# Kernel tuning notes

Measured on AMD Instinct MI355X. Metric: run time of the kernel, lower is better.

The kernel has to match this reference:

```python
import jax, jax.numpy as jnp
import numpy as np

K = 1023   # kernel_size == embedding_dim
H = 16     # out_channels (filters per sample)
E = 256    # num_embeddings
T = 8      # num_tokens
CC = 0.25  # commitment cost
EPS = np.float32(np.finfo(np.float32).eps)
DN = ('NCH', 'OIH', 'NCH')


def setup_inputs() -> dict:
    key = jax.random.key(0)
    ks = jax.random.split(key, 10)
    B, C, L = 8, 1, 8184
    D_ff = 2 * E
    X = jax.random.normal(ks[0], (B, C, L), jnp.float32)
    embedding = jax.random.uniform(ks[1], (E, K), jnp.float32, -1.0 / E, 1.0 / E)
    ffn_w1 = jax.random.normal(ks[2], (E, D_ff), jnp.float32) * 0.02
    ffn_b1 = jnp.zeros((D_ff,), jnp.float32)
    ffn_w2 = jax.random.normal(ks[3], (D_ff, E), jnp.float32) * 0.02
    ffn_b2 = jnp.zeros((E,), jnp.float32)
    ln_g = jnp.ones((E,), jnp.float32)
    ln_b = jnp.zeros((E,), jnp.float32)
    cls_w = jax.random.normal(ks[4], (E, 10), jnp.float32) * 0.02
    cls_b = jnp.zeros((10,), jnp.float32)
    return dict(X=X, embedding=embedding, ffn_w1=ffn_w1, ffn_b1=ffn_b1,
                ffn_w2=ffn_w2, ffn_b2=ffn_b2, ln_g=ln_g, ln_b=ln_b,
                cls_w=cls_w, cls_b=cls_b)


def _autocov(f):
    # f: [..., K]. FFT-based autocovariance of hann-windowed, max-normalized frame.
    n = f.shape[-1]
    fmax = jnp.max(jnp.abs(f), axis=-1, keepdims=True)
    fmax = jnp.where(fmax == 0, EPS, fmax)
    win = 0.5 * (1.0 - jnp.cos(2.0 * jnp.pi * jnp.arange(n, dtype=jnp.float32) / n))
    xw = f * win / fmax
    spec = jnp.abs(jnp.fft.rfft(xw, n=n) ** 2)   # |rfft(x)^2| == |rfft(x)|^2
    return jnp.fft.ifftshift(jnp.fft.irfft(spec, n=n), axes=-1)


def reference(X, embedding, ffn_w1, ffn_b1, ffn_w2, ffn_b2, ln_g, ln_b, cls_w, cls_b):
    B, C, L = X.shape
    # ---- encoder: extract frames at fixed linspace positions, autocovariance ----
    Lp = ((L + K - 1) // K) * K          # PadForConv(zero) length (no-op here)
    end = Lp - K - 1 - K
    positions = jnp.linspace(0.0, float(end), H).astype(jnp.int32)
    idx = positions[:, None] + jnp.arange(K)          # (H, K)
    frames = X[:, :, idx]                             # (B, C, H, K) gather
    Z = _autocov(jnp.transpose(frames, (0, 2, 1, 3)))  # (B, H, C, K)
    # ---- VQ: pairwise distances + argmin + codebook lookup ----
    flat = Z.reshape(-1, K)                           # (B*H*C, K)
    d = (jnp.sum(flat ** 2, axis=1, keepdims=True)
         + jnp.sum(embedding ** 2, axis=1)
         - 2.0 * flat @ embedding.T)                  # (B*H*C, E)
    codes = jnp.argmin(d, axis=1)
    enc = jax.nn.one_hot(codes, E, dtype=flat.dtype)
    quant = (enc @ embedding).reshape(Z.shape)
    sg = jax.lax.stop_gradient
    e_loss = jnp.mean((sg(quant) - Z) ** 2)
    q_loss = jnp.mean((quant - sg(Z)) ** 2)
    vq_loss = q_loss + CC * e_loss
    quant_st = Z + sg(quant - Z)                      # straight-through
    avg = jnp.mean(enc, axis=0)
    perplexity = jnp.exp(-jnp.sum(avg * jnp.log(avg + EPS)))
    # ---- decoder: every sample's filter bank convolved with the whole batch ----
    fmerged = quant_st.reshape(B * H, C, K)           # merge per-sample banks
    out = jax.lax.conv_general_dilated(X, fmerged, (1,), 'SAME',
                                       dimension_numbers=DN)  # (B, B*H, L)
    out = out.reshape(B, B, H, L)                     # (batch b, filter-sample i, k, L)
    sq = (out - X[:, None, :, :]) ** 2                # C==1 broadcast
    # sum_i mean_k mse_{b,l} == mean over (b,k,l) then sum over i
    recon_loss = jnp.sum(jnp.mean(sq, axis=(0, 2, 3)))
    # ---- project: conv with codebook as filters ----
    pfilt = jnp.broadcast_to(embedding[:, None, :], (E, C, K))
    proj = jax.lax.conv_general_dilated(X, pfilt, (1,), 'VALID',
                                        dimension_numbers=DN)  # (B, E, Lo)
    Lo = proj.shape[-1]
    pad = ((Lo + T - 1) // T) * T - Lo                # PadForConv(mean)
    m = jnp.mean(proj, axis=-1, keepdims=True)
    proj = jnp.concatenate([proj, jnp.broadcast_to(m, (B, E, pad))], axis=-1)
    # ---- classify ----
    x = proj.reshape(B, E, T, -1).transpose(0, 2, 3, 1)  # (B, T, t, E)
    x = jnp.max(x, axis=2)                               # (B, T, E)
    mu = jnp.mean(x, axis=-1, keepdims=True)
    var = jnp.var(x, axis=-1, keepdims=True)
    xn = (x - mu) / jnp.sqrt(var + 1e-5) * ln_g + ln_b
    hdd = jax.nn.relu(xn @ ffn_w1 + ffn_b1) @ ffn_w2 + ffn_b2
    feat = jnp.mean(hdd, axis=1)                         # (B, E)
    logits = feat @ cls_w + cls_b
    return (logits, vq_loss, recon_loss, perplexity)
```

## Files before the change

kernel.cpp:

```cpp
#include <hip/hip_runtime.h>

#define KK 1023
#define LL 8184
#define LO 7162
#define XPS 10240
#define EPSF 1.1920928955078125e-07f
#define NEG_INF (-3.4028234663852886e+38f)

typedef short bf16x8 __attribute__((ext_vector_type(8)));
typedef float f32x4 __attribute__((ext_vector_type(4)));

__device__ __constant__ int c_pos[16] = {0,409,818,1227,1636,2045,2454,2863,
                                         3273,3682,4091,4500,4909,5318,5727,6137};

__device__ __forceinline__ unsigned short f2bf(float f) {
    unsigned u = __float_as_uint(f);
    unsigned r = (u + 0x7FFFu + ((u >> 16) & 1u)) >> 16;
    return (unsigned short)r;
}
__device__ __forceinline__ int fenc(float f) {
    int u = __float_as_int(f);
    return u >= 0 ? u : (~u) ^ 0x80000000;
}
__device__ __forceinline__ float fdec(int k) {
    int u = k >= 0 ? k : ~(k ^ 0x80000000);
    return __int_as_float(u);
}
__device__ __forceinline__ void gl2lds16(const void* g, void* l) {
    __builtin_amdgcn_global_load_lds(
        (const __attribute__((address_space(1))) void*)g,
        (__attribute__((address_space(3))) void*)l, 16, 0, 0);
}

__global__ __launch_bounds__(256) void k_pa(const float* __restrict__ X,
                                            const float* __restrict__ emb,
                                            unsigned short* __restrict__ Xpad,
                                            unsigned short* __restrict__ Xodd,
                                            unsigned short* __restrict__ Ebf,
                                            float* __restrict__ Etf,
                                            float* __restrict__ enorm,
                                            int* __restrict__ hist,
                                            int* __restrict__ cmax,
                                            float* __restrict__ Z) {
    __shared__ __align__(16) float xw[2048];
    __shared__ float red[256];
    const int q = blockIdx.x;
    const int tid = threadIdx.x;
    if (q < 256) {
        const int fi = q >> 1, half = q & 1;
        const int b = fi >> 4, h = fi & 15;
        const float* xp = X + b * LL + c_pos[h];
        float lmax = 0.f;
        for (int j = tid; j < KK; j += 256) {
            float v = xp[j];
            xw[j] = v;
            lmax = fmaxf(lmax, fabsf(v));
        }
        red[tid] = lmax;
        __syncthreads();
        for (int off = 128; off; off >>= 1) {
            if (tid < off) red[tid] = fmaxf(red[tid], red[tid + off]);
            __syncthreads();
        }
        float fmx = red[0];
        if (fmx == 0.f) fmx = EPSF;
        __syncthreads();
        for (int j = tid; j < KK; j += 256) {
            float v = xw[j];
            float win = 0.5f * (1.0f - cosf(6.28318530717958647692f * (float)j / 1023.0f));
            float w = v * win / fmx;
            xw[j] = w;
            xw[j + KK] = w;
        }
        __syncthreads();

        if (tid < 128) {
            const int m = half * 512 + 4 * tid;
            const int mh = m >> 1;
            const int mq4 = mh >> 1;
            const float2* X2 = (const float2*)xw;
            const float4* X4 = (const float4*)xw;
            float a0 = 0.f, a1 = 0.f, a2 = 0.f, a3 = 0.f;
            float2 W0 = X2[mh], W1 = X2[mh + 1], W2 = X2[mh + 2], W3 = X2[mh + 3];
            for (int jh = 0; jh < 510; jh += 2) {
                float4 nw = X4[mq4 + (jh >> 1) + 2];
                float4 xj = X4[jh >> 1];
                a0 = fmaf(xj.x, W0.x, a0);
                a0 = fmaf(xj.y, W0.y, a0);
                a0 = fmaf(xj.z, W1.x, a0);
                a0 = fmaf(xj.w, W1.y, a0);
                a1 = fmaf(xj.x, W0.y, a1);
                a1 = fmaf(xj.y, W1.x, a1);
                a1 = fmaf(xj.z, W1.y, a1);
                a1 = fmaf(xj.w, W2.x, a1);
                a2 = fmaf(xj.x, W1.x, a2);
                a2 = fmaf(xj.y, W1.y, a2);
                a2 = fmaf(xj.z, W2.x, a2);
                a2 = fmaf(xj.w, W2.y, a2);
                a3 = fmaf(xj.x, W1.y, a3);
                a3 = fmaf(xj.y, W2.x, a3);
                a3 = fmaf(xj.z, W2.y, a3);
                a3 = fmaf(xj.w, W3.x, a3);
                W0 = W2; W1 = W3;
                W2 = make_float2(nw.x, nw.y);
                W3 = make_float2(nw.z, nw.w);
            }
            {
                float2 xj = X2[510];
                a0 = fmaf(xj.x, W0.x, a0);
                a0 = fmaf(xj.y, W0.y, a0);
                a1 = fmaf(xj.x, W0.y, a1);
                a1 = fmaf(xj.y, W1.x, a1);
                a2 = fmaf(xj.x, W1.x, a2);
                a2 = fmaf(xj.y, W1.y, a2);
                a3 = fmaf(xj.x, W1.y, a3);
                a3 = fmaf(xj.y, W2.x, a3);
            }
            float xt = xw[1022];
            a0 = fmaf(xt, W1.x, a0);
            a1 = fmaf(xt, W1.y, a1);
            a2 = fmaf(xt, W2.x, a2);
            a3 = fmaf(xt, W2.y, a3);

            float* zrow = Z + fi * KK;
            float av[4] = {a0, a1, a2, a3};
#pragma unroll
            for (int qq = 0; qq < 4; ++qq) {
                int mmq = m + qq;
                if (mmq < KK) {
                    int i0 = mmq + 512; if (i0 >= KK) i0 -= KK;
                    zrow[i0] = av[qq];
                }
            }
        }
    } else if (q < 288) {
        const int qq = q - 256;
        const int b = qq >> 2, seg = qq & 3;
        for (int i = seg * 2560 + tid; i < (seg + 1) * 2560; i += 256) {
            unsigned short v = 0, vo = 0;
            if (i >= 512 && i < 512 + LL) v = f2bf(X[b * LL + (i - 512)]);
            const int i1 = i + 1;
            if (i1 >= 512 && i1 < 512 + LL) vo = f2bf(X[b * LL + (i1 - 512)]);
            Xpad[b * XPS + i] = v;
            Xodd[b * XPS + i] = vo;
        }
    } else if (q < 544) {
        const int e = q - 288;
        const float* er = emb + e * KK;
        float nrm = 0.f;
        for (int k = tid; k < 1024; k += 256) {
            float v = (k < KK) ? er[k] : 0.f;
            Ebf[e * 1024 + k] = (k < KK) ? f2bf(v) : (unsigned short)0;
            Etf[(k >> 2) * 1024 + e * 4 + (k & 3)] = v;
            nrm = fmaf(v, v, nrm);
        }
        red[tid] = nrm;
        __syncthreads();
        for (int off = 128; off; off >>= 1) {
            if (tid < off) red[tid] += red[tid + off];
            __syncthreads();
        }
        if (tid == 0) enorm[e] = red[0];
    } else {
        const int i = (q - 544) * 256 + tid;
        cmax[i] = INT_MIN;
        if (q == 544) hist[tid] = 0;
    }
}

__global__ __launch_bounds__(256, 4) void kA(const float* __restrict__ Z,
                                             const float4* __restrict__ Et4,
                                             const float* __restrict__ enorm,
                                             const float* __restrict__ emb,
                                             int* __restrict__ codes,
                                             int* __restrict__ hist,
                                             float* __restrict__ vq_part,
                                             const unsigned short* __restrict__ Xpad,
                                             const unsigned short* __restrict__ Xodd,
                                             const unsigned short* __restrict__ Ebf,
                                             float* __restrict__ psum_part,
                                             int* __restrict__ cmax) {
    __shared__ __align__(16) char smem[29696];
    const int tid = threadIdx.x;
    const int bi = blockIdx.x;
    if (bi < 128) {
        float* zl  = (float*)smem;
        float* zm2 = (float*)(smem + 4096);
        float* rv  = (float*)(smem + 8192);
        int*   ri  = (int*)(smem + 9216);
        const int fi = bi;
        const float* zrow = Z + fi * KK;
        for (int t = tid; t < 1024; t += 256) {
            float z = (t < KK) ? zrow[t] : 0.f;
            if (t < KK) zl[t] = z;
            zm2[t] = -2.f * z;
        }
        __syncthreads();

        float d = enorm[tid];
        const float4* zp = (const float4*)zm2;
        const float4* ep = Et4 + tid;
#pragma unroll 8
        for (int t4 = 0; t4 < 256; ++t4) {
            float4 ev = ep[t4 * 256];
            float4 zv = zp[t4];
            d = fmaf(zv.x, ev.x, d);
            d = fmaf(zv.y, ev.y, d);
            d = fmaf(zv.z, ev.z, d);
            d = fmaf(zv.w, ev.w, d);
        }
        rv[tid] = d; ri[tid] = tid;
        __syncthreads();
        for (int off = 128; off; off >>= 1) {
            if (tid < off) {
                float v2 = rv[tid + off]; int i2 = ri[tid + off];
                if (v2 < rv[tid] || (v2 == rv[tid] && i2 < ri[tid])) { rv[tid] = v2; ri[tid] = i2; }
            }
            __syncthreads();
        }
        const int code = ri[0];
        if (tid == 0) { codes[fi] = code; atomicAdd(&hist[code], 1); }

        const float* qr = emb + code * KK;
        float s = 0.f;
        for (int t = tid; t < KK; t += 256) { float dd = qr[t] - zl[t]; s += dd * dd; }
        __syncthreads();
        rv[tid] = s;
        __syncthreads();
        for (int off = 128; off; off >>= 1) {
            if (tid < off) rv[tid] += rv[tid + off];
            __syncthreads();
        }
        if (tid == 0) vq_part[fi] = rv[0];
        return;
    }
    unsigned short* lds_b = (unsigned short*)smem;
    unsigned short* lds_a = (unsigned short*)(smem + 20480);
    float (*red_s)[4] = (float(*)[4])(smem + 28672);
    const int lane = tid & 63;
    const int c = lane & 15, g = lane >> 4;
    const int wg = tid >> 6;

    const int pb = bi - 128;
    const int b = pb / 112;
    const int r = pb % 112;
    const int row0 = (r / 28) * 64;
    const int l0 = (r % 28) * 256;
    const int xw0 = 512 + l0;

    {
        const unsigned short* base_e = Xpad + b * XPS + xw0;
        const unsigned short* base_o = Xodd + b * XPS + xw0;
        for (int k = tid; k < 1280; k += 256) {
            const int wdw = k / 160;
            const int p = k - wdw * 160;
            const unsigned short* src = (wdw & 1) ? (base_o + wdw - 1 + p * 8)
                                                  : (base_e + wdw + p * 8);
            gl2lds16(src, lds_b + k * 8);
        }
    }
    const int r_lds = tid >> 2, q4 = tid & 3;
    const unsigned short* e_src = Ebf + (row0 + r_lds) * 1024 + q4 * 8;
    gl2lds16(e_src, lds_a + tid * 8);
    __syncthreads();

    f32x4 acc[4][4];
#pragma unroll
    for (int i = 0; i < 4; ++i)
#pragma unroll
        for (int j = 0; j < 4; ++j) acc[i][j] = (f32x4){0.f, 0.f, 0.f, 0.f};

    const char* lax = (const char*)lds_a;
    const char* lbx = (const char*)lds_b;
    const int boff0 = (wg & 1) * 10240 + ((wg >> 1) << 4) + 32 * c + 16 * g;
    const int aoff0 = c * 64 + g * 16;

    for (int s = 0; s < 32; ++s) {
        const int cur = s & 1;
        if (s + 1 < 32)
            gl2lds16(e_src + (s + 1) * 32, lds_a + ((s + 1) & 1) * 2048 + tid * 8);
        const char* ab = lax + cur * 4096 + aoff0;
        bf16x8 af[4];
#pragma unroll
        for (int et = 0; et < 4; ++et) af[et] = *(const bf16x8*)(ab + et * 1024);
#pragma unroll
        for (int ntl = 0; ntl < 4; ++ntl) {
            bf16x8 bfrag = *(const bf16x8*)(lbx + boff0 + ntl * 2560 + 64 * s);
#pragma unroll
            for (int et = 0; et < 4; ++et)
                acc[et][ntl] = __builtin_amdgcn_mfma_f32_16x16x32_bf16(af[et], bfrag, acc[et][ntl], 0, 0, 0);
        }
        __syncthreads();
    }

    const int lseg  = l0 >> 8;
    const int lbase = l0 + wg * 4;
    const int ch0 = lbase / 896;
#pragma unroll
    for (int et = 0; et < 4; ++et) {
#pragma unroll
        for (int r4 = 0; r4 < 4; ++r4) {
            float ssum = 0.f, m0 = NEG_INF, m1 = NEG_INF;
#pragma unroll
            for (int ntl = 0; ntl < 4; ++ntl) {
                float v = acc[et][ntl][r4];
                int l = lbase + ntl + 16 * c;
                bool ok = l < LO;
                ssum += ok ? v : 0.f;
                int ch = l / 896;
                if (ok && ch == ch0) m0 = fmaxf(m0, v);
                if (ok && ch != ch0) m1 = fmaxf(m1, v);
            }
            ssum += __shfl_xor(ssum, 1); ssum += __shfl_xor(ssum, 2);
            ssum += __shfl_xor(ssum, 4); ssum += __shfl_xor(ssum, 8);
            m0 = fmaxf(m0, __shfl_xor(m0, 1)); m0 = fmaxf(m0, __shfl_xor(m0, 2));
            m0 = fmaxf(m0, __shfl_xor(m0, 4)); m0 = fmaxf(m0, __shfl_xor(m0, 8));
            m1 = fmaxf(m1, __shfl_xor(m1, 1)); m1 = fmaxf(m1, __shfl_xor(m1, 2));
            m1 = fmaxf(m1, __shfl_xor(m1, 4)); m1 = fmaxf(m1, __shfl_xor(m1, 8));
            if (c == 0) {
                int eidx = et * 16 + g * 4 + r4;
                red_s[eidx][wg] = ssum;
                int e = row0 + eidx;
                int cb = (b * 256 + e) * 8;
                if (m0 > NEG_INF && ch0 < 8)     atomicMax(&cmax[cb + ch0], fenc(m0));
                if (m1 > NEG_INF && ch0 + 1 < 8) atomicMax(&cmax[cb + ch0 + 1], fenc(m1));
            }
        }
    }
    __syncthreads();
    if (tid < 64) {
        float tot = red_s[tid][0] + red_s[tid][1] + red_s[tid][2] + red_s[tid][3];
        psum_part[lseg * 2048 + b * 256 + row0 + tid] = tot;
    }
}

__global__ __launch_bounds__(256, 4) void kB(const float* __restrict__ psum_part,
                                             const int* __restrict__ cmax,
                                             const float* __restrict__ ln_g,
                                             const float* __restrict__ ln_b,
                                             const float* __restrict__ w1,
                                             const float* __restrict__ b1,
                                             float* __restrict__ hbuf,
                                             const unsigned short* __restrict__ Xpad,
                                             const unsigned short* __restrict__ Xodd,
                                             const unsigned short* __restrict__ Ebf,
                                             const int* __restrict__ codes,
                                             const float* __restrict__ X,
                                             float* __restrict__ recon_part) {
    __shared__ __align__(16) char smem[29696];
    const int tid = threadIdx.x;
    const int bi = blockIdx.x;
    if (bi < 64) {
        float* red  = (float*)smem;
        float* red2 = (float*)(smem + 1024);
        float* xr   = (float*)(smem + 2048);
        const int bt = bi;
        const int t = bt & 7;
        const int b = bt >> 3;
        const int e = tid;
        const float* ps = psum_part + b * 256 + e;
        float sm = 0.f;
#pragma unroll
        for (int s = 0; s < 28; ++s) sm += ps[s * 2048];
        float m = sm * (1.0f / 7162.0f);
        const int cb = (b * 256 + e) << 3;
        float v = (t < 7) ? fdec(cmax[cb + t]) : fmaxf(fdec(cmax[cb + 7]), m);
        red[e] = v; red2[e] = v * v;
        __syncthreads();
        for (int off = 128; off; off >>= 1) {
            if (e < off) { red[e] += red[e + off]; red2[e] += red2[e + off]; }
            __syncthreads();
        }
        float mu  = red[0] * (1.0f / 256.0f);
        float var = red2[0] * (1.0f / 256.0f) - mu * mu;
        float rr = 1.0f / sqrtf(var + 1e-5f);
        xr[e] = (v - mu) * rr * ln_g[e] + ln_b[e];
        __syncthreads();

        float a0 = 0.f, a1 = 0.f;
#pragma unroll 4
        for (int ee = 0; ee < 256; ++ee) {
            float xv = xr[ee];
            a0 = fmaf(xv, w1[ee * 512 + e], a0);
            a1 = fmaf(xv, w1[ee * 512 + 256 + e], a1);
        }
        hbuf[bt * 512 + e]       = fmaxf(a0 + b1[e], 0.f);
        hbuf[bt * 512 + 256 + e] = fmaxf(a1 + b1[256 + e], 0.f);
        return;
    }
    unsigned short* lds_b = (unsigned short*)smem;
    unsigned short* lds_a = (unsigned short*)(smem + 20480);
    float (*red_s)[4] = (float(*)[4])(smem + 28672);
    const int lane = tid & 63;
    const int c = lane & 15, g = lane >> 4;
    const int wg = tid >> 6;

    const int rb = bi - 64;
    const int b = rb >> 6;
    const int r = rb & 63;
    const int row0 = (r >> 5) * 64;
    const int l0 = (r & 31) * 256;
    const int xw0 = l0;

    {
        const unsigned short* base_e = Xpad + b * XPS + xw0;
        const unsigned short* base_o = Xodd + b * XPS + xw0;
        for (int k = tid; k < 1280; k += 256) {
            const int wdw = k / 160;
            const int p = k - wdw * 160;
            const unsigned short* src = (wdw & 1) ? (base_o + wdw - 1 + p * 8)
                                                  : (base_e + wdw + p * 8);
            gl2lds16(src, lds_b + k * 8);
        }
    }
    const int r_lds = tid >> 2, q4 = tid & 3;
    const unsigned short* e_src = Ebf + codes[row0 + r_lds] * 1024 + q4 * 8;
    gl2lds16(e_src, lds_a + tid * 8);
    __syncthreads();

    f32x4 acc[4][4];
#pragma unroll
    for (int i = 0; i < 4; ++i)
#pragma unroll
        for (int j = 0; j < 4; ++j) acc[i][j] = (f32x4){0.f, 0.f, 0.f, 0.f};

    const char* lax = (const char*)lds_a;
    const char* lbx = (const char*)lds_b;
    const int boff0 = (wg & 1) * 10240 + ((wg >> 1) << 4) + 32 * c + 16 * g;
    const int aoff0 = c * 64 + g * 16;

    for (int s = 0; s < 32; ++s) {
        const int cur = s & 1;
        if (s + 1 < 32)
            gl2lds16(e_src + (s + 1) * 32, lds_a + ((s + 1) & 1) * 2048 + tid * 8);
        const char* ab = lax + cur * 4096 + aoff0;
        bf16x8 af[4];
#pragma unroll
        for (int et = 0; et < 4; ++et) af[et] = *(const bf16x8*)(ab + et * 1024);
#pragma unroll
        for (int ntl = 0; ntl < 4; ++ntl) {
            bf16x8 bfrag = *(const bf16x8*)(lbx + boff0 + ntl * 2560 + 64 * s);
#pragma unroll
            for (int et = 0; et < 4; ++et)
                acc[et][ntl] = __builtin_amdgcn_mfma_f32_16x16x32_bf16(af[et], bfrag, acc[et][ntl], 0, 0, 0);
        }
        __syncthreads();
    }

    const int lseg  = l0 >> 8;
    const int lbase = l0 + wg * 4;
    float xv[4];
#pragma unroll
    for (int ntl = 0; ntl < 4; ++ntl) {
        int lr = lbase + ntl + 16 * c - 1;
        xv[ntl] = (lr >= 0 && lr < LL) ? X[b * LL + lr] : 0.f;
    }
#pragma unroll
    for (int et = 0; et < 4; ++et) {
#pragma unroll
        for (int r4 = 0; r4 < 4; ++r4) {
            float ssum = 0.f;
#pragma unroll
            for (int ntl = 0; ntl < 4; ++ntl) {
                int lr = lbase + ntl + 16 * c - 1;
                bool ok = (lr >= 0) && (lr < LL);
                float dd = ok ? (acc[et][ntl][r4] - xv[ntl]) : 0.f;
                ssum += dd * dd;
            }
            ssum += __shfl_xor(ssum, 1); ssum += __shfl_xor(ssum, 2);
            ssum += __shfl_xor(ssum, 4); ssum += __shfl_xor(ssum, 8);
            if (c == 0) red_s[et * 16 + g * 4 + r4][wg] = ssum;
        }
    }
    __syncthreads();
    if (tid < 64) {
        float tot = red_s[tid][0] + red_s[tid][1] + red_s[tid][2] + red_s[tid][3];
        recon_part[(b * 128 + row0 + tid) * 32 + lseg] = tot;
    }
}

__global__ __launch_bounds__(256) void kC(const float* __restrict__ hbuf,
                                          const float* __restrict__ w2,
                                          const float* __restrict__ b2,
                                          float* __restrict__ hdd,
                                          const float* __restrict__ recon_part,
                                          const float* __restrict__ vq_part,
                                          const int* __restrict__ hist,
                                          float* __restrict__ out) {
    __shared__ __align__(16) char smem[3072];
    const int tid = threadIdx.x;
    const int bi = blockIdx.x;
    if (bi < 256) {
        float* hr = (float*)smem;
        float* rv = (float*)(smem + 2048);
        const int bt = bi & 63, jc = bi >> 6;
        hr[tid] = hbuf[bt * 512 + tid];
        hr[tid + 256] = hbuf[bt * 512 + 256 + tid];
        __syncthreads();
        const int jj = tid & 63, ks = tid >> 6;
        const int e = jc * 64 + jj;
        const float* wp = w2 + (ks * 128) * 256 + e;
        float a = 0.f;
#pragma unroll
        for (int j = 0; j < 128; ++j) a = fmaf(hr[ks * 128 + j], wp[j * 256], a);
        rv[tid] = a;
        __syncthreads();
        if (tid < 64) {
            float s = rv[tid] + rv[tid + 64] + rv[tid + 128] + rv[tid + 192];
            hdd[bt * 256 + jc * 64 + tid] = s + b2[jc * 64 + tid];
        }
    } else {
        float* red = (float*)smem;
        float s = 0.f;
        for (int i = tid; i < 32768; i += 256) s += recon_part[i];
        red[tid] = s;
        __syncthreads();
        for (int off = 128; off; off >>= 1) { if (tid < off) red[tid] += red[tid + off]; __syncthreads(); }
        if (tid == 0) out[81] = red[0] / 1047552.0f;
        __syncthreads();
        red[tid] = (tid < 128) ? vq_part[tid] : 0.f;
        __syncthreads();
        for (int off = 128; off; off >>= 1) { if (tid < off) red[tid] += red[tid + off]; __syncthreads(); }
        if (tid == 0) out[80] = 1.25f * red[0] / 130944.0f;
        __syncthreads();
        float avg = (float)hist[tid] * (1.0f / 128.0f);
        red[tid] = avg * logf(avg + EPSF);
        __syncthreads();
        for (int off = 128; off; off >>= 1) { if (tid < off) red[tid] += red[tid + off]; __syncthreads(); }
        if (tid == 0) out[82] = expf(-red[0]);
    }
}

__global__ __launch_bounds__(256) void kD(const float* __restrict__ hdd,
                                          const float* __restrict__ cls_w,
                                          const float* __restrict__ cls_b,
                                          float* __restrict__ out) {
    __shared__ float feat[8][256];
    const int tid = threadIdx.x;
#pragma unroll
    for (int b2 = 0; b2 < 8; ++b2) {
        float fb = 0.f;
#pragma unroll
        for (int t2 = 0; t2 < 8; ++t2) fb += hdd[(b2 * 8 + t2) * 256 + tid];
        feat[b2][tid] = fb * 0.125f;
    }
    __syncthreads();
    if (tid < 80) {
        const int b = tid / 10, k = tid % 10;
        float a = cls_b[k];
        for (int e = 0; e < 256; ++e) a = fmaf(feat[b][e], cls_w[e * 10 + k], a);
        out[tid] = a;
    }
}

extern "C" void kernel_launch(void* const* d_in, const int* in_sizes, int n_in,
                              void* d_out, int out_size, void* d_ws, size_t ws_size,
                              hipStream_t stream) {
    const float* X     = (const float*)d_in[0];
    const float* emb   = (const float*)d_in[1];
    const float* w1    = (const float*)d_in[2];
    const float* b1    = (const float*)d_in[3];
    const float* w2    = (const float*)d_in[4];
    const float* b2    = (const float*)d_in[5];
    const float* ln_g  = (const float*)d_in[6];
    const float* ln_b  = (const float*)d_in[7];
    const float* cls_w = (const float*)d_in[8];
    const float* cls_b = (const float*)d_in[9];
    float* out = (float*)d_out;

    float* Z            = (float*)d_ws;
    float* vq_part      = Z + 130944;
    float* xnbuf        = vq_part + 128;
    float* hdd          = xnbuf + 16384;
    float* psum_part    = hdd + 16384;
    float* recon_part   = psum_part + 65536;
    int*   cmaxb        = (int*)(recon_part + 32768);
    int*   codes        = cmaxb + 16384;
    int*   hist         = codes + 128;
    unsigned short* Xpad = (unsigned short*)(hist + 256);
    unsigned short* Xodd = Xpad + 8 * XPS;
    unsigned short* Ebf  = Xodd + 8 * XPS;
    float* Etf           = (float*)(Ebf + 256 * 1024);
    float* enorm         = Etf + 256 * 1024;
    float* hbuf          = enorm + 256;

    k_pa<<<dim3(608), dim3(256), 0, stream>>>(X, emb, Xpad, Xodd, Ebf, Etf, enorm, hist, cmaxb, Z);
    kA  <<<dim3(1024), dim3(256), 0, stream>>>(Z, (const float4*)Etf, enorm, emb, codes, hist,
                                               vq_part, Xpad, Xodd, Ebf, psum_part, cmaxb);
    kB  <<<dim3(576), dim3(256), 0, stream>>>(psum_part, cmaxb, ln_g, ln_b, w1, b1, hbuf,
                                              Xpad, Xodd, Ebf, codes, X, recon_part);
    kC  <<<dim3(257), dim3(256), 0, stream>>>(hbuf, w2, b2, hdd, recon_part, vq_part, hist, out);
    kD  <<<dim3(1),   dim3(256), 0, stream>>>(hdd, cls_w, cls_b, out);
}
```

Baseline: 122.4 us.

## Give each wave a private A-tile buffer to drop per-step block barriers

Each of the four waves now loads and double-buffers its own copy of the 64-row codebook A tile in LDS. The MFMA K-loop then waits on the wave's own loads with s_waitcnt vmcnt instead of a block-wide __syncthreads every step, and the last step is peeled out of the loop. The aim is to remove 32 block barriers per tile and let waves run out of step with each other. In exchange, LDS per block rises from about 29 KB to 52 KB, occupancy hints drop from 4 to 3 blocks per CU, and every wave fetches the same A data four times, raising load traffic.

After: 135.5 us. +10.7%, slower.

```diff
diff --git a/kernel.cpp b/kernel.cpp
--- a/kernel.cpp
+++ b/kernel.cpp
@@ -168,7 +168,7 @@
     }
 }
 
-__global__ __launch_bounds__(256, 4) void kA(const float* __restrict__ Z,
+__global__ __launch_bounds__(256, 3) void kA(const float* __restrict__ Z,
                                              const float4* __restrict__ Et4,
                                              const float* __restrict__ enorm,
                                              const float* __restrict__ emb,
@@ -180,7 +180,7 @@
                                              const unsigned short* __restrict__ Ebf,
                                              float* __restrict__ psum_part,
                                              int* __restrict__ cmax) {
-    __shared__ __align__(16) char smem[29696];
+    __shared__ __align__(16) char smem[53248];
     const int tid = threadIdx.x;
     const int bi = blockIdx.x;
     if (bi < 128) {
@@ -235,11 +235,10 @@
         return;
     }
     unsigned short* lds_b = (unsigned short*)smem;
-    unsigned short* lds_a = (unsigned short*)(smem + 20480);
-    float (*red_s)[4] = (float(*)[4])(smem + 28672);
     const int lane = tid & 63;
     const int c = lane & 15, g = lane >> 4;
     const int wg = tid >> 6;
+    unsigned short* Aw = (unsigned short*)(smem + 20480) + wg * 4096;
 
     const int pb = bi - 128;
     const int b = pb / 112;
@@ -259,9 +258,14 @@
             gl2lds16(src, lds_b + k * 8);
         }
     }
-    const int r_lds = tid >> 2, q4 = tid & 3;
-    const unsigned short* e_src = Ebf + (row0 + r_lds) * 1024 + q4 * 8;
-    gl2lds16(e_src, lds_a + tid * 8);
+    const unsigned short* asrc[4];
+#pragma unroll
+    for (int i = 0; i < 4; ++i) {
+        const int rr = i * 16 + (lane >> 2);
+        asrc[i] = Ebf + (row0 + rr) * 1024 + (lane & 3) * 8;
+    }
+#pragma unroll
+    for (int i = 0; i < 4; ++i) gl2lds16(asrc[i], Aw + i * 512 + lane * 8);
     __syncthreads();
 
     f32x4 acc[4][4];
@@ -270,15 +274,18 @@
 #pragma unroll
         for (int j = 0; j < 4; ++j) acc[i][j] = (f32x4){0.f, 0.f, 0.f, 0.f};
 
-    const char* lax = (const char*)lds_a;
+    const char* lax = (const char*)Aw;
     const char* lbx = (const char*)lds_b;
     const int boff0 = (wg & 1) * 10240 + ((wg >> 1) << 4) + 32 * c + 16 * g;
     const int aoff0 = c * 64 + g * 16;
 
-    for (int s = 0; s < 32; ++s) {
+    for (int s = 0; s < 31; ++s) {
         const int cur = s & 1;
-        if (s + 1 < 32)
-            gl2lds16(e_src + (s + 1) * 32, lds_a + ((s + 1) & 1) * 2048 + tid * 8);
+        unsigned short* dst = Aw + (cur ^ 1) * 2048;
+#pragma unroll
+        for (int i = 0; i < 4; ++i) gl2lds16(asrc[i] + (s + 1) * 32, dst + i * 512 + lane * 8);
+        asm volatile("s_waitcnt vmcnt(4)" ::: "memory");
+        __builtin_amdgcn_sched_barrier(0);
         const char* ab = lax + cur * 4096 + aoff0;
         bf16x8 af[4];
 #pragma unroll
@@ -290,8 +297,24 @@
             for (int et = 0; et < 4; ++et)
                 acc[et][ntl] = __builtin_amdgcn_mfma_f32_16x16x32_bf16(af[et], bfrag, acc[et][ntl], 0, 0, 0);
         }
-        __syncthreads();
-    }
+    }
+    {
+        asm volatile("s_waitcnt vmcnt(0)" ::: "memory");
+        __builtin_amdgcn_sched_barrier(0);
+        const char* ab = lax + 4096 + aoff0;
+        bf16x8 af[4];
+#pragma unroll
+        for (int et = 0; et < 4; ++et) af[et] = *(const bf16x8*)(ab + et * 1024);
+#pragma unroll
+        for (int ntl = 0; ntl < 4; ++ntl) {
+            bf16x8 bfrag = *(const bf16x8*)(lbx + boff0 + ntl * 2560 + 64 * 31);
+#pragma unroll
+            for (int et = 0; et < 4; ++et)
+                acc[et][ntl] = __builtin_amdgcn_mfma_f32_16x16x32_bf16(af[et], bfrag, acc[et][ntl], 0, 0, 0);
+        }
+    }
+    __syncthreads();
+    float (*red_s)[4] = (float(*)[4])smem;
 
     const int lseg  = l0 >> 8;
     const int lbase = l0 + wg * 4;
@@ -334,7 +357,7 @@
     }
 }
 
-__global__ __launch_bounds__(256, 4) void kB(const float* __restrict__ psum_part,
+__global__ __launch_bounds__(256, 3) void kB(const float* __restrict__ psum_part,
                                              const int* __restrict__ cmax,
                                              const float* __restrict__ ln_g,
                                              const float* __restrict__ ln_b,
@@ -347,7 +370,7 @@
                                              const int* __restrict__ codes,
                                              const float* __restrict__ X,
                                              float* __restrict__ recon_part) {
-    __shared__ __align__(16) char smem[29696];
+    __shared__ __align__(16) char smem[53248];
     const int tid = threadIdx.x;
     const int bi = blockIdx.x;
     if (bi < 64) {
@@ -389,11 +412,10 @@
         return;
     }
     unsigned short* lds_b = (unsigned short*)smem;
-    unsigned short* lds_a = (unsigned short*)(smem + 20480);
-    float (*red_s)[4] = (float(*)[4])(smem + 28672);
     const int lane = tid & 63;
     const int c = lane & 15, g = lane >> 4;
     const int wg = tid >> 6;
+    unsigned short* Aw = (unsigned short*)(smem + 20480) + wg * 4096;
 
     const int rb = bi - 64;
     const int b = rb >> 6;
@@ -413,9 +435,14 @@
             gl2lds16(src, lds_b + k * 8);
         }
     }
-    const int r_lds = tid >> 2, q4 = tid & 3;
-    const unsigned short* e_src = Ebf + codes[row0 + r_lds] * 1024 + q4 * 8;
-    gl2lds16(e_src, lds_a + tid * 8);
+    const unsigned short* asrc[4];
+#pragma unroll
+    for (int i = 0; i < 4; ++i) {
+        const int rr = i * 16 + (lane >> 2);
+        asrc[i] = Ebf + codes[row0 + rr] * 1024 + (lane & 3) * 8;
+    }
+#pragma unroll
+    for (int i = 0; i < 4; ++i) gl2lds16(asrc[i], Aw + i * 512 + lane * 8);
     __syncthreads();
 
     f32x4 acc[4][4];
@@ -424,15 +451,18 @@
 #pragma unroll
         for (int j = 0; j < 4; ++j) acc[i][j] = (f32x4){0.f, 0.f, 0.f, 0.f};
 
-    const char* lax = (const char*)lds_a;
+    const char* lax = (const char*)Aw;
     const char* lbx = (const char*)lds_b;
     const int boff0 = (wg & 1) * 10240 + ((wg >> 1) << 4) + 32 * c + 16 * g;
     const int aoff0 = c * 64 + g * 16;
 
-    for (int s = 0; s < 32; ++s) {
+    for (int s = 0; s < 31; ++s) {
         const int cur = s & 1;
-        if (s + 1 < 32)
-            gl2lds16(e_src + (s + 1) * 32, lds_a + ((s + 1) & 1) * 2048 + tid * 8);
+        unsigned short* dst = Aw + (cur ^ 1) * 2048;
+#pragma unroll
+        for (int i = 0; i < 4; ++i) gl2lds16(asrc[i] + (s + 1) * 32, dst + i * 512 + lane * 8);
+        asm volatile("s_waitcnt vmcnt(4)" ::: "memory");
+        __builtin_amdgcn_sched_barrier(0);
         const char* ab = lax + cur * 4096 + aoff0;
         bf16x8 af[4];
 #pragma unroll
@@ -444,8 +474,24 @@
             for (int et = 0; et < 4; ++et)
                 acc[et][ntl] = __builtin_amdgcn_mfma_f32_16x16x32_bf16(af[et], bfrag, acc[et][ntl], 0, 0, 0);
         }
-        __syncthreads();
-    }
+    }
+    {
+        asm volatile("s_waitcnt vmcnt(0)" ::: "memory");
+        __builtin_amdgcn_sched_barrier(0);
+        const char* ab = lax + 4096 + aoff0;
+        bf16x8 af[4];
+#pragma unroll
+        for (int et = 0; et < 4; ++et) af[et] = *(const bf16x8*)(ab + et * 1024);
+#pragma unroll
+        for (int ntl = 0; ntl < 4; ++ntl) {
+            bf16x8 bfrag = *(const bf16x8*)(lbx + boff0 + ntl * 2560 + 64 * 31);
+#pragma unroll
+            for (int et = 0; et < 4; ++et)
+                acc[et][ntl] = __builtin_amdgcn_mfma_f32_16x16x32_bf16(af[et], bfrag, acc[et][ntl], 0, 0, 0);
+        }
+    }
+    __syncthreads();
+    float (*red_s)[4] = (float(*)[4])smem;
 
     const int lseg  = l0 >> 8;
     const int lbase = l0 + wg * 4;
```
